# Kernel optimization log

Hardware: AMD Instinct MI355X
Metric: run time of the kernel (lower is better)

## Reference

```python
import jax, jax.numpy as jnp
import numpy as np

N = 50000      # nodes
E = 500000     # edges
D_IN, D_HID, D_OUT = 128, 128, 64


def setup_inputs() -> dict:
    key = jax.random.key(0)
    ks = jax.random.split(key, 9)
    x = jax.random.normal(ks[0], (N, D_IN), dtype=jnp.float32)
    edge_index = jax.random.randint(ks[1], (2, E), 0, N, dtype=jnp.int64)
    s1 = 1.0 / np.sqrt(D_IN)
    s2 = 1.0 / np.sqrt(D_HID)
    W1 = jax.random.normal(ks[2], (D_IN, D_HID), dtype=jnp.float32) * s1
    b1 = jnp.zeros((D_HID,), dtype=jnp.float32)
    W2 = jax.random.normal(ks[3], (D_HID, D_HID), dtype=jnp.float32) * s2
    b2 = jnp.zeros((D_HID,), dtype=jnp.float32)
    W3 = jax.random.normal(ks[4], (D_HID, D_OUT), dtype=jnp.float32) * s2
    b3 = jnp.zeros((D_OUT,), dtype=jnp.float32)
    return {"x": x, "edge_index": edge_index,
            "W1": W1, "b1": b1, "W2": W2, "b2": b2, "W3": W3, "b3": b3}


def _gcn_norm(edge_index, num_nodes):
    # PyG GCNConv default: add self loops, symmetric normalization.
    loop = jnp.arange(num_nodes, dtype=edge_index.dtype)
    src = jnp.concatenate([edge_index[0], loop])  # [E+N]
    dst = jnp.concatenate([edge_index[1], loop])
    deg = jax.ops.segment_sum(jnp.ones_like(dst, dtype=jnp.float32), dst,
                              num_segments=num_nodes)
    dinv = jnp.where(deg > 0, jax.lax.rsqrt(deg), 0.0)
    norm = dinv[src] * dinv[dst]  # [E+N]
    return src, dst, norm


def _gcn_conv(x, W, b, src, dst, norm, num_nodes):
    # linear transform then degree-normalized scatter-add aggregation
    h = x @ W                                 # [N, F_out]
    msg = h[src] * norm[:, None]              # gather + scale  [E+N, F_out]
    out = jax.ops.segment_sum(msg, dst, num_segments=num_nodes)
    return out + b


def reference(x, edge_index, W1, b1, W2, b2, W3, b3):
    src, dst, norm = _gcn_norm(edge_index, N)
    h = _gcn_conv(x, W1, b1, src, dst, norm, N)
    h = _gcn_conv(h, W2, b2, src, dst, norm, N)
    h = _gcn_conv(h, W3, b3, src, dst, norm, N)
    return h
```

## Files before the change

kernel.cpp:

```cpp
#include <hip/hip_runtime.h>

#define DIN 128
#define DHID 128
#define DOUT 64

__device__ __forceinline__ float bf2f(ushort u) {
  return __uint_as_float(((unsigned)u) << 16);
}
__device__ __forceinline__ ushort f2bf(float f) {
  unsigned u = __float_as_uint(f);
  return (ushort)((u + 0x7fffu + ((u >> 16) & 1u)) >> 16);
}


__global__ void k_init(int* counts, int* cursor, int n) {
  int i = blockIdx.x * blockDim.x + threadIdx.x;
  if (i < n) { counts[i] = 0; cursor[i] = 0; }
}

__global__ void k_hist(const int* __restrict__ ei, int E, int* __restrict__ counts) {
  int e = blockIdx.x * blockDim.x + threadIdx.x;
  if (e < E) atomicAdd(&counts[ei[E + e]], 1);
}

__global__ void k_dinv(const int* __restrict__ counts, float* __restrict__ dinv, int n) {
  int i = blockIdx.x * blockDim.x + threadIdx.x;
  if (i < n) dinv[i] = 1.0f / sqrtf((float)(counts[i] + 1));
}

__global__ __launch_bounds__(1024) void k_scan1(const int* __restrict__ counts,
                                                int* __restrict__ rowptr,
                                                int* __restrict__ bsums, int n) {
  __shared__ int s[1024];
  int tid = threadIdx.x;
  int idx = blockIdx.x * 1024 + tid;
  int v = (idx < n) ? counts[idx] : 0;
  s[tid] = v;
  __syncthreads();
  for (int off = 1; off < 1024; off <<= 1) {
    int t = (tid >= off) ? s[tid - off] : 0;
    __syncthreads();
    s[tid] += t;
    __syncthreads();
  }
  if (idx < n) rowptr[idx] = s[tid] - v;
  if (tid == 1023) bsums[blockIdx.x] = s[1023];
}

__global__ void k_scan2(int* bsums, int nb) {
  int l = threadIdx.x;
  if (nb <= 64) {
    int v = (l < nb) ? bsums[l] : 0;
    int orig = v;
    for (int off = 1; off < 64; off <<= 1) {
      int t = __shfl_up(v, off);
      if (l >= off) v += t;
    }
    if (l < nb) bsums[l] = v - orig;
  } else if (l == 0) {
    int run = 0;
    for (int b = 0; b < nb; ++b) { int v = bsums[b]; bsums[b] = run; run += v; }
  }
}

__global__ __launch_bounds__(1024) void k_scan3(int* __restrict__ rowptr,
                                                const int* __restrict__ bsums, int n, int E) {
  int idx = blockIdx.x * 1024 + threadIdx.x;
  if (idx < n) rowptr[idx] += bsums[blockIdx.x];
  if (idx == 0) rowptr[n] = E;
}

__global__ void k_scatter(const int* __restrict__ ei, int E,
                          const int* __restrict__ rowptr, int* __restrict__ cursor,
                          int* __restrict__ csrc) {
  int e = blockIdx.x * blockDim.x + threadIdx.x;
  if (e >= E) return;
  int s = ei[e];
  int d = ei[E + e];
  int pos = rowptr[d] + atomicAdd(&cursor[d], 1);
  csrc[pos] = s;
}


template <int NCOL>
__global__ void k_mmnaive(const float* __restrict__ A, const float* __restrict__ B,
                          float* __restrict__ C) {
  int t = blockIdx.x * blockDim.x + threadIdx.x;
  if (t >= 128 * NCOL) return;
  int i = t / NCOL, j = t % NCOL;
  float s = 0.f;
  for (int k = 0; k < 128; ++k) s = fmaf(A[i * 128 + k], B[k * NCOL + j], s);
  C[t] = s;
}

__global__ void k_cvec(const float* __restrict__ b1, const float* __restrict__ b2,
                       const float* __restrict__ b3, const float* __restrict__ W2,
                       const float* __restrict__ W3, float* __restrict__ c1,
                       float* __restrict__ c2, float* __restrict__ c3) {
  __shared__ float t1[DHID];
  int j = threadIdx.x;
  float s = 0.f;
  for (int k = 0; k < DHID; ++k) s = fmaf(b1[k], W2[k * DHID + j], s);
  t1[j] = s;
  __syncthreads();
  if (j < DOUT) {
    float a = 0.f, b = 0.f;
    for (int k = 0; k < DHID; ++k) {
      a = fmaf(t1[k], W3[k * DOUT + j], a);
      b = fmaf(b2[k], W3[k * DOUT + j], b);
    }
    c1[j] = a; c2[j] = b; c3[j] = b3[j];
  }
}


__global__ __launch_bounds__(256) void k_xw(const float* __restrict__ X,
                                            const float* __restrict__ Wc,
                                            ushort* __restrict__ H, int n,
                                            int c0, int W) {
  __shared__ float Xs[64][68];
  __shared__ float Ws[64][64];
  int t = threadIdx.x;
  int br = blockIdx.x * 64;
  int r4 = t >> 4, c4 = t & 15;
  float4 acc[4];
#pragma unroll
  for (int i = 0; i < 4; ++i) acc[i] = make_float4(0.f, 0.f, 0.f, 0.f);

  for (int chunk = 0; chunk < 2; ++chunk) {
    int k0 = chunk * 64;
    __syncthreads();
#pragma unroll
    for (int j = 0; j < 4; ++j) {
      int f4 = t + j * 256;
      int row = f4 >> 4, col4 = f4 & 15;
      int gr = br + row;
      float4 v = make_float4(0.f, 0.f, 0.f, 0.f);
      if (gr < n) v = *(const float4*)&X[(size_t)gr * DIN + k0 + col4 * 4];
      *(float4*)&Xs[row][col4 * 4] = v;
      float4 w = *(const float4*)&Wc[(size_t)(k0 + row) * DOUT + col4 * 4];
      *(float4*)&Ws[row][col4 * 4] = w;
    }
    __syncthreads();
#pragma unroll
    for (int kk = 0; kk < 16; ++kk) {
      float4 xv[4], wv[4];
#pragma unroll
      for (int i = 0; i < 4; ++i) xv[i] = *(const float4*)&Xs[r4 * 4 + i][kk * 4];
#pragma unroll
      for (int q = 0; q < 4; ++q) wv[q] = *(const float4*)&Ws[kk * 4 + q][c4 * 4];
#pragma unroll
      for (int i = 0; i < 4; ++i) {
        acc[i].x = fmaf(xv[i].x, wv[0].x, acc[i].x);
        acc[i].y = fmaf(xv[i].x, wv[0].y, acc[i].y);
        acc[i].z = fmaf(xv[i].x, wv[0].z, acc[i].z);
        acc[i].w = fmaf(xv[i].x, wv[0].w, acc[i].w);
        acc[i].x = fmaf(xv[i].y, wv[1].x, acc[i].x);
        acc[i].y = fmaf(xv[i].y, wv[1].y, acc[i].y);
        acc[i].z = fmaf(xv[i].y, wv[1].z, acc[i].z);
        acc[i].w = fmaf(xv[i].y, wv[1].w, acc[i].w);
        acc[i].x = fmaf(xv[i].z, wv[2].x, acc[i].x);
        acc[i].y = fmaf(xv[i].z, wv[2].y, acc[i].y);
        acc[i].z = fmaf(xv[i].z, wv[2].z, acc[i].z);
        acc[i].w = fmaf(xv[i].z, wv[2].w, acc[i].w);
        acc[i].x = fmaf(xv[i].w, wv[3].x, acc[i].x);
        acc[i].y = fmaf(xv[i].w, wv[3].y, acc[i].y);
        acc[i].z = fmaf(xv[i].w, wv[3].z, acc[i].z);
        acc[i].w = fmaf(xv[i].w, wv[3].w, acc[i].w);
      }
    }
  }
#pragma unroll
  for (int i = 0; i < 4; ++i) {
    int gr = br + r4 * 4 + i;
    int col = c4 * 4;
    if (gr < n && col >= c0 && col < c0 + W) {
      ushort4 hv;
      hv.x = f2bf(acc[i].x); hv.y = f2bf(acc[i].y);
      hv.z = f2bf(acc[i].z); hv.w = f2bf(acc[i].w);
      *(ushort4*)&H[(size_t)gr * W + (col - c0)] = hv;
    }
  }
}


template <int ROUND>
__global__ __launch_bounds__(256) void k_agg(const ushort* __restrict__ hin, int hs,
                                             ushort* __restrict__ ho16,
                                             float* __restrict__ ho32, int ho,
                                             const int* __restrict__ rowptr,
                                             const int* __restrict__ csrc,
                                             const float* __restrict__ dinv,
                                             float* __restrict__ r1, float* __restrict__ r2,
                                             const float* __restrict__ c1,
                                             const float* __restrict__ c2,
                                             const float* __restrict__ c3,
                                             int n, int W, int wsh, int c0, int pass0) {
  int id = blockIdx.x * blockDim.x + threadIdx.x;
  int node = id >> wsh;
  if (node >= n) return;
  int feat = id & (W - 1);
  int beg = rowptr[node], end = rowptr[node + 1];
  float di = dinv[node];
  float a0 = 0.f, a1 = 0.f, a2 = 0.f, a3 = 0.f, racc = 0.f;
  bool doR = (ROUND != 3) && pass0;
  int e = beg;
  for (; e + 4 <= end; e += 4) {
    int s0 = csrc[e], s1 = csrc[e + 1], s2 = csrc[e + 2], s3 = csrc[e + 3];
    float w0 = dinv[s0] * di, w1 = dinv[s1] * di;
    float w2 = dinv[s2] * di, w3 = dinv[s3] * di;
    float h0 = bf2f(hin[(size_t)s0 * hs + feat]);
    float h1 = bf2f(hin[(size_t)s1 * hs + feat]);
    float h2 = bf2f(hin[(size_t)s2 * hs + feat]);
    float h3 = bf2f(hin[(size_t)s3 * hs + feat]);
    a0 = fmaf(w0, h0, a0); a1 = fmaf(w1, h1, a1);
    a2 = fmaf(w2, h2, a2); a3 = fmaf(w3, h3, a3);
    if (doR) {
      if (ROUND == 1) racc += (w0 + w1) + (w2 + w3);
      if (ROUND == 2) {
        racc = fmaf(w0, r1[s0], racc); racc = fmaf(w1, r1[s1], racc);
        racc = fmaf(w2, r1[s2], racc); racc = fmaf(w3, r1[s3], racc);
      }
    }
  }
  for (; e < end; ++e) {
    int s = csrc[e];
    float w = dinv[s] * di;
    a0 = fmaf(w, bf2f(hin[(size_t)s * hs + feat]), a0);
    if (doR) {
      if (ROUND == 1) racc += w;
      if (ROUND == 2) racc = fmaf(w, r1[s], racc);
    }
  }
  float acc = (a0 + a1) + (a2 + a3);
  float d2 = di * di;
  acc = fmaf(d2, bf2f(hin[(size_t)node * hs + feat]), acc);
  if (ROUND == 1 && doR) { racc += d2; if (feat == 0) r1[node] = racc; }
  if (ROUND == 2 && doR) { racc = fmaf(d2, r1[node], racc); if (feat == 0) r2[node] = racc; }
  if (ROUND == 3) {
    int cf = c0 + feat;
    acc = fmaf(r2[node], c1[cf], acc);
    acc = fmaf(r1[node], c2[cf], acc);
    acc += c3[cf];
    ho32[(size_t)node * ho + feat] = acc;
  } else {
    ho16[(size_t)node * hs + feat] = f2bf(acc);
  }
}


extern "C" void kernel_launch(void* const* d_in, const int* in_sizes, int n_in,
                              void* d_out, int out_size, void* d_ws, size_t ws_size,
                              hipStream_t stream) {
  const float* X  = (const float*)d_in[0];
  const int*   ei = (const int*)d_in[1];
  const float* W1 = (const float*)d_in[2];
  const float* b1 = (const float*)d_in[3];
  const float* W2 = (const float*)d_in[4];
  const float* b2 = (const float*)d_in[5];
  const float* W3 = (const float*)d_in[6];
  const float* b3 = (const float*)d_in[7];
  const int N = in_sizes[0] / DIN;
  const int E = in_sizes[1] / 2;
  float* out = (float*)d_out;

  auto AL = [](size_t x) -> size_t { return (x + 255) & ~(size_t)255; };

  size_t fixedBytes = AL((size_t)(N + 1) * 4)
                    + AL(256 * 4)
                    + AL((size_t)N * 4)
                    + AL((size_t)E * 4)
                    + AL((size_t)N * 4)
                    + AL((size_t)N * 4)
                    + AL((size_t)DIN * DHID * 4)
                    + AL((size_t)DIN * DOUT * 4)
                    + 3 * AL(DOUT * 4);
  int npass = 1;
  while (npass < 8 && fixedBytes + 2 * AL((size_t)N * (DOUT / npass) * 2) > ws_size)
    npass <<= 1;
  const int W = DOUT / npass;
  int wsh = 0; while ((1 << wsh) < W) ++wsh;

  char* p = (char*)d_ws;
  auto alloc = [&](size_t nbytes) -> void* {
    void* r = (void*)p;
    p += AL(nbytes);
    return r;
  };
  int*    rowptr = (int*)alloc((size_t)(N + 1) * 4);
  int*    bsums  = (int*)alloc(256 * 4);
  float*  dinv   = (float*)alloc((size_t)N * 4);
  int*    csrc   = (int*)alloc((size_t)E * 4);
  int*    counts = (int*)alloc((size_t)N * 4);
  int*    cursor = (int*)alloc((size_t)N * 4);
  float*  wtmp   = (float*)alloc((size_t)DIN * DHID * 4);
  float*  wc     = (float*)alloc((size_t)DIN * DOUT * 4);
  float*  c1     = (float*)alloc(DOUT * 4);
  float*  c2     = (float*)alloc(DOUT * 4);
  float*  c3     = (float*)alloc(DOUT * 4);
  ushort* H1     = (ushort*)alloc((size_t)N * W * 2);
  ushort* H2     = (ushort*)alloc((size_t)N * W * 2);
  float*  r1     = (float*)counts;
  float*  r2     = (float*)cursor;

  k_init<<<(N + 255) / 256, 256, 0, stream>>>(counts, cursor, N);
  k_hist<<<(E + 255) / 256, 256, 0, stream>>>(ei, E, counts);
  k_dinv<<<(N + 255) / 256, 256, 0, stream>>>(counts, dinv, N);
  int nb = (N + 1023) / 1024;
  k_scan1<<<nb, 1024, 0, stream>>>(counts, rowptr, bsums, N);
  k_scan2<<<1, 64, 0, stream>>>(bsums, nb);
  k_scan3<<<nb, 1024, 0, stream>>>(rowptr, bsums, N, E);
  k_scatter<<<(E + 255) / 256, 256, 0, stream>>>(ei, E, rowptr, cursor, csrc);

  k_mmnaive<128><<<(128 * 128 + 255) / 256, 256, 0, stream>>>(W1, W2, wtmp);
  k_mmnaive<64><<<(128 * 64 + 255) / 256, 256, 0, stream>>>(wtmp, W3, wc);
  k_cvec<<<1, 128, 0, stream>>>(b1, b2, b3, W2, W3, c1, c2, c3);

  for (int pp = 0; pp < npass; ++pp) {
    int c0 = pp * W;
    int pass0 = (pp == 0) ? 1 : 0;
    k_xw<<<(N + 63) / 64, 256, 0, stream>>>(X, wc, H1, N, c0, W);
    int gb = (int)(((size_t)N * W + 255) / 256);
    k_agg<1><<<gb, 256, 0, stream>>>(H1, W, H2, nullptr, DOUT, rowptr, csrc, dinv,
                                     r1, r2, c1, c2, c3, N, W, wsh, c0, pass0);
    k_agg<2><<<gb, 256, 0, stream>>>(H2, W, H1, nullptr, DOUT, rowptr, csrc, dinv,
                                     r1, r2, c1, c2, c3, N, W, wsh, c0, pass0);
    k_agg<3><<<gb, 256, 0, stream>>>(H1, W, nullptr, out + c0, DOUT, rowptr, csrc, dinv,
                                     r1, r2, c1, c2, c3, N, W, wsh, c0, 0);
  }
}
```

Measured before the change: 200.6 us.

## Compute XW once into slice-major buffer and fold dinv scaling into features

Computes X·Wc once for all output columns, storing it as dinv-prescaled bf16 slices in slice-major layout, instead of recomputing the GEMM for every column pass. The aggregation kernels then sum pre-scaled neighbor values without a per-edge dinv gather and multiply. The bias-propagation terms are reformulated to match. Edge-index and CSR loads become nontemporal loads. Slice width now defaults to 32 columns, so a second aggregation pass runs where the old code might have used one, and more workspace is needed for the full H buffer.

```diff
diff --git a/kernel.cpp b/kernel.cpp
--- a/kernel.cpp
+++ b/kernel.cpp
@@ -20,7 +20,7 @@
 
 __global__ void k_hist(const int* __restrict__ ei, int E, int* __restrict__ counts) {
   int e = blockIdx.x * blockDim.x + threadIdx.x;
-  if (e < E) atomicAdd(&counts[ei[E + e]], 1);
+  if (e < E) atomicAdd(&counts[__builtin_nontemporal_load(ei + E + e)], 1);
 }
 
 __global__ void k_dinv(const int* __restrict__ counts, float* __restrict__ dinv, int n) {
@@ -75,8 +75,8 @@
                           int* __restrict__ csrc) {
   int e = blockIdx.x * blockDim.x + threadIdx.x;
   if (e >= E) return;
-  int s = ei[e];
-  int d = ei[E + e];
+  int s = __builtin_nontemporal_load(ei + e);
+  int d = __builtin_nontemporal_load(ei + E + e);
   int pos = rowptr[d] + atomicAdd(&cursor[d], 1);
   csrc[pos] = s;
 }
@@ -116,8 +116,8 @@
 
 __global__ __launch_bounds__(256) void k_xw(const float* __restrict__ X,
                                             const float* __restrict__ Wc,
-                                            ushort* __restrict__ H, int n,
-                                            int c0, int W) {
+                                            const float* __restrict__ dinv,
+                                            ushort* __restrict__ Hs, int n, int W) {
   __shared__ float Xs[64][68];
   __shared__ float Ws[64][64];
   int t = threadIdx.x;
@@ -173,25 +173,28 @@
 #pragma unroll
   for (int i = 0; i < 4; ++i) {
     int gr = br + r4 * 4 + i;
-    int col = c4 * 4;
-    if (gr < n && col >= c0 && col < c0 + W) {
+    if (gr < n) {
+      float dv = dinv[gr];
+      int col = c4 * 4;
+      int p = col / W, off = col - p * W;
       ushort4 hv;
-      hv.x = f2bf(acc[i].x); hv.y = f2bf(acc[i].y);
-      hv.z = f2bf(acc[i].z); hv.w = f2bf(acc[i].w);
-      *(ushort4*)&H[(size_t)gr * W + (col - c0)] = hv;
+      hv.x = f2bf(acc[i].x * dv); hv.y = f2bf(acc[i].y * dv);
+      hv.z = f2bf(acc[i].z * dv); hv.w = f2bf(acc[i].w * dv);
+      *(ushort4*)&Hs[((size_t)p * n + gr) * W + off] = hv;
     }
   }
 }
 
 
 template <int ROUND>
-__global__ __launch_bounds__(256) void k_agg(const ushort* __restrict__ hin, int hs,
-                                             ushort* __restrict__ ho16,
-                                             float* __restrict__ ho32, int ho,
+__global__ __launch_bounds__(256) void k_agg(const ushort* __restrict__ in,
+                                             ushort* __restrict__ out16,
+                                             float* __restrict__ out32,
                                              const int* __restrict__ rowptr,
                                              const int* __restrict__ csrc,
                                              const float* __restrict__ dinv,
-                                             float* __restrict__ r1, float* __restrict__ r2,
+                                             float* __restrict__ r1t, float* __restrict__ r1s,
+                                             float* __restrict__ r2t,
                                              const float* __restrict__ c1,
                                              const float* __restrict__ c2,
                                              const float* __restrict__ c3,
@@ -206,45 +209,45 @@
   bool doR = (ROUND != 3) && pass0;
   int e = beg;
   for (; e + 4 <= end; e += 4) {
-    int s0 = csrc[e], s1 = csrc[e + 1], s2 = csrc[e + 2], s3 = csrc[e + 3];
-    float w0 = dinv[s0] * di, w1 = dinv[s1] * di;
-    float w2 = dinv[s2] * di, w3 = dinv[s3] * di;
-    float h0 = bf2f(hin[(size_t)s0 * hs + feat]);
-    float h1 = bf2f(hin[(size_t)s1 * hs + feat]);
-    float h2 = bf2f(hin[(size_t)s2 * hs + feat]);
-    float h3 = bf2f(hin[(size_t)s3 * hs + feat]);
-    a0 = fmaf(w0, h0, a0); a1 = fmaf(w1, h1, a1);
-    a2 = fmaf(w2, h2, a2); a3 = fmaf(w3, h3, a3);
+    int s0 = __builtin_nontemporal_load(csrc + e);
+    int s1 = __builtin_nontemporal_load(csrc + e + 1);
+    int s2 = __builtin_nontemporal_load(csrc + e + 2);
+    int s3 = __builtin_nontemporal_load(csrc + e + 3);
+    float h0 = bf2f(in[(size_t)s0 * W + feat]);
+    float h1 = bf2f(in[(size_t)s1 * W + feat]);
+    float h2 = bf2f(in[(size_t)s2 * W + feat]);
+    float h3 = bf2f(in[(size_t)s3 * W + feat]);
+    a0 += h0; a1 += h1; a2 += h2; a3 += h3;
     if (doR) {
-      if (ROUND == 1) racc += (w0 + w1) + (w2 + w3);
-      if (ROUND == 2) {
-        racc = fmaf(w0, r1[s0], racc); racc = fmaf(w1, r1[s1], racc);
-        racc = fmaf(w2, r1[s2], racc); racc = fmaf(w3, r1[s3], racc);
-      }
+      if (ROUND == 1) racc += (dinv[s0] + dinv[s1]) + (dinv[s2] + dinv[s3]);
+      if (ROUND == 2) racc += (r1s[s0] + r1s[s1]) + (r1s[s2] + r1s[s3]);
     }
   }
   for (; e < end; ++e) {
-    int s = csrc[e];
-    float w = dinv[s] * di;
-    a0 = fmaf(w, bf2f(hin[(size_t)s * hs + feat]), a0);
+    int s = __builtin_nontemporal_load(csrc + e);
+    a0 += bf2f(in[(size_t)s * W + feat]);
     if (doR) {
-      if (ROUND == 1) racc += w;
-      if (ROUND == 2) racc = fmaf(w, r1[s], racc);
-    }
-  }
-  float acc = (a0 + a1) + (a2 + a3);
+      if (ROUND == 1) racc += dinv[s];
+      if (ROUND == 2) racc += r1s[s];
+    }
+  }
+  float T = ((a0 + a1) + (a2 + a3)) + bf2f(in[(size_t)node * W + feat]);
   float d2 = di * di;
-  acc = fmaf(d2, bf2f(hin[(size_t)node * hs + feat]), acc);
-  if (ROUND == 1 && doR) { racc += d2; if (feat == 0) r1[node] = racc; }
-  if (ROUND == 2 && doR) { racc = fmaf(d2, r1[node], racc); if (feat == 0) r2[node] = racc; }
+  if (ROUND == 1 && doR) {
+    racc += di;
+    if (feat == 0) { r1t[node] = di * racc; r1s[node] = d2 * racc; }
+  }
+  if (ROUND == 2 && doR) {
+    racc += r1s[node];
+    if (feat == 0) r2t[node] = di * racc;
+  }
   if (ROUND == 3) {
     int cf = c0 + feat;
-    acc = fmaf(r2[node], c1[cf], acc);
-    acc = fmaf(r1[node], c2[cf], acc);
-    acc += c3[cf];
-    ho32[(size_t)node * ho + feat] = acc;
+    float v = fmaf(r1t[node], c2[cf], c3[cf]);
+    v = fmaf(r2t[node], c1[cf], v);
+    out32[(size_t)node * DOUT + cf] = fmaf(di, T, v);
   } else {
-    ho16[(size_t)node * hs + feat] = f2bf(acc);
+    out16[(size_t)node * W + feat] = f2bf(d2 * T);
   }
 }
 
@@ -266,19 +269,13 @@
 
   auto AL = [](size_t x) -> size_t { return (x + 255) & ~(size_t)255; };
 
-  size_t fixedBytes = AL((size_t)(N + 1) * 4)
-                    + AL(256 * 4)
-                    + AL((size_t)N * 4)
-                    + AL((size_t)E * 4)
-                    + AL((size_t)N * 4)
-                    + AL((size_t)N * 4)
-                    + AL((size_t)DIN * DHID * 4)
-                    + AL((size_t)DIN * DOUT * 4)
-                    + 3 * AL(DOUT * 4);
-  int npass = 1;
-  while (npass < 8 && fixedBytes + 2 * AL((size_t)N * (DOUT / npass) * 2) > ws_size)
-    npass <<= 1;
-  const int W = DOUT / npass;
+  size_t fixedBytes = AL((size_t)(N + 1) * 4) + AL(256 * 4) + AL((size_t)N * 4) * 4
+                    + AL((size_t)E * 4) + AL((size_t)DIN * DHID * 4)
+                    + AL((size_t)DIN * DOUT * 4) + 3 * AL(DOUT * 4);
+  int W = 32;
+  while (W > 8 && fixedBytes + AL((size_t)N * DOUT * 2) + AL((size_t)N * W * 2) > ws_size)
+    W >>= 1;
+  const int SLICES = DOUT / W;
   int wsh = 0; while ((1 << wsh) < W) ++wsh;
 
   char* p = (char*)d_ws;
@@ -293,15 +290,16 @@
   int*    csrc   = (int*)alloc((size_t)E * 4);
   int*    counts = (int*)alloc((size_t)N * 4);
   int*    cursor = (int*)alloc((size_t)N * 4);
+  float*  r2t    = (float*)alloc((size_t)N * 4);
   float*  wtmp   = (float*)alloc((size_t)DIN * DHID * 4);
   float*  wc     = (float*)alloc((size_t)DIN * DOUT * 4);
   float*  c1     = (float*)alloc(DOUT * 4);
   float*  c2     = (float*)alloc(DOUT * 4);
   float*  c3     = (float*)alloc(DOUT * 4);
-  ushort* H1     = (ushort*)alloc((size_t)N * W * 2);
-  ushort* H2     = (ushort*)alloc((size_t)N * W * 2);
-  float*  r1     = (float*)counts;
-  float*  r2     = (float*)cursor;
+  ushort* Hfull  = (ushort*)alloc((size_t)N * DOUT * 2);
+  ushort* S1     = (ushort*)alloc((size_t)N * W * 2);
+  float*  r1t    = (float*)counts;
+  float*  r1s    = (float*)cursor;
 
   k_init<<<(N + 255) / 256, 256, 0, stream>>>(counts, cursor, N);
   k_hist<<<(E + 255) / 256, 256, 0, stream>>>(ei, E, counts);
@@ -316,16 +314,18 @@
   k_mmnaive<64><<<(128 * 64 + 255) / 256, 256, 0, stream>>>(wtmp, W3, wc);
   k_cvec<<<1, 128, 0, stream>>>(b1, b2, b3, W2, W3, c1, c2, c3);
 
-  for (int pp = 0; pp < npass; ++pp) {
+  k_xw<<<(N + 63) / 64, 256, 0, stream>>>(X, wc, dinv, Hfull, N, W);
+
+  for (int pp = 0; pp < SLICES; ++pp) {
     int c0 = pp * W;
     int pass0 = (pp == 0) ? 1 : 0;
-    k_xw<<<(N + 63) / 64, 256, 0, stream>>>(X, wc, H1, N, c0, W);
+    ushort* Hp = Hfull + (size_t)pp * N * W;
     int gb = (int)(((size_t)N * W + 255) / 256);
-    k_agg<1><<<gb, 256, 0, stream>>>(H1, W, H2, nullptr, DOUT, rowptr, csrc, dinv,
-                                     r1, r2, c1, c2, c3, N, W, wsh, c0, pass0);
-    k_agg<2><<<gb, 256, 0, stream>>>(H2, W, H1, nullptr, DOUT, rowptr, csrc, dinv,
-                                     r1, r2, c1, c2, c3, N, W, wsh, c0, pass0);
-    k_agg<3><<<gb, 256, 0, stream>>>(H1, W, nullptr, out + c0, DOUT, rowptr, csrc, dinv,
-                                     r1, r2, c1, c2, c3, N, W, wsh, c0, 0);
-  }
-}
+    k_agg<1><<<gb, 256, 0, stream>>>(Hp, S1, nullptr, rowptr, csrc, dinv,
+                                     r1t, r1s, r2t, c1, c2, c3, N, W, wsh, c0, pass0);
+    k_agg<2><<<gb, 256, 0, stream>>>(S1, Hp, nullptr, rowptr, csrc, dinv,
+                                     r1t, r1s, r2t, c1, c2, c3, N, W, wsh, c0, pass0);
+    k_agg<3><<<gb, 256, 0, stream>>>(Hp, nullptr, out, rowptr, csrc, dinv,
+                                     r1t, r1s, r2t, c1, c2, c3, N, W, wsh, c0, 0);
+  }
+}
```

Result: slower. 237.5 us (+18.4%).
